# Kernel tuning notes

Measured on AMD Instinct MI355X. Metric: run time of the kernel, lower is better.

The kernel has to match this reference:

```python
import jax, jax.numpy as jnp
import numpy as np


def setup_inputs() -> dict:
    key = jax.random.key(0)
    inputs = jax.random.normal(key, (4096, 8192), dtype=jnp.float32)
    return {"inputs": inputs, "k": 512}


def reference(inputs, k):
    # Original: kth_smallest = sort_ascending(inputs)[..., n-1-k]
    # i.e. the (k+1)-th largest value per row. Equivalent via top_k.
    # Keep only elements STRICTLY greater than that threshold.
    thresh = jax.lax.top_k(inputs, k + 1)[0][..., -1]  # [batch]
    mask = (inputs > thresh[:, None]).astype(inputs.dtype)
    return inputs * mask
```

## Files before the change

kernel.cpp:

```cpp
#include <hip/hip_runtime.h>
#include <stdint.h>


constexpr int COLS = 8192;
constexpr int TPB  = 256;
constexpr int EPT  = COLS / TPB;
constexpr int VPT  = EPT / 4;
constexpr int HIST_STRIDE = 260;

__device__ __forceinline__ uint32_t map_f32(uint32_t u) {
  return (u & 0x80000000u) ? ~u : (u | 0x80000000u);
}

__device__ __forceinline__ float unmap_f32(uint32_t m) {
  return __uint_as_float((m & 0x80000000u) ? (m ^ 0x80000000u) : ~m);
}

__global__ __launch_bounds__(TPB)
void ksparse_kernel(const float* __restrict__ in, const int* __restrict__ kptr,
                    float* __restrict__ out) {
  __shared__ uint32_t hist[4 * HIST_STRIDE];
  __shared__ uint32_t sscan[256];
  __shared__ uint32_t wtot[4];
  __shared__ int s_dmax;

  const int t    = threadIdx.x;
  const int wave = t >> 6;
  const int lane = t & 63;
  const size_t rowbase = (size_t)blockIdx.x * COLS;

  uint32_t m[EPT];
  const float4* inp = (const float4*)(in + rowbase);
#pragma unroll
  for (int i = 0; i < VPT; ++i) {
    float4 v = inp[t + i * TPB];
    m[4 * i + 0] = map_f32(__float_as_uint(v.x));
    m[4 * i + 1] = map_f32(__float_as_uint(v.y));
    m[4 * i + 2] = map_f32(__float_as_uint(v.z));
    m[4 * i + 3] = map_f32(__float_as_uint(v.w));
  }

  uint32_t kk = (uint32_t)(*kptr) + 1u;
  uint32_t prefix = 0;

#pragma unroll 1
  for (int pass = 0; pass < 4; ++pass) {
    const int shift = 24 - 8 * pass;

#pragma unroll
    for (int j = 0; j < 5; ++j) {
      int idx = t + j * TPB;
      if (idx < 4 * HIST_STRIDE) hist[idx] = 0u;
    }
    if (t == 0) s_dmax = -1;
    __syncthreads();

    const uint32_t hi_mask = (pass == 0) ? 0u : (0xFFFFFFFFu << (shift + 8));
    const uint32_t want    = (pass == 0) ? 0u : (prefix << (shift + 8));
    uint32_t* h = &hist[wave * HIST_STRIDE];
#pragma unroll
    for (int i = 0; i < EPT; ++i) {
      if ((m[i] & hi_mask) == want)
        atomicAdd(&h[(m[i] >> shift) & 255u], 1u);
    }
    __syncthreads();

    uint32_t s = hist[t] + hist[HIST_STRIDE + t] +
                 hist[2 * HIST_STRIDE + t] + hist[3 * HIST_STRIDE + t];
#pragma unroll
    for (int off = 1; off < 64; off <<= 1) {
      uint32_t tmp = __shfl_down(s, off, 64);
      s += (lane + off < 64) ? tmp : 0u;
    }
    if (lane == 0) wtot[wave] = s;
    __syncthreads();

    uint32_t suff = s;
#pragma unroll
    for (int w = 1; w < 4; ++w)
      if (w > wave) suff += wtot[w];
    sscan[t] = suff;
    if (suff >= kk) atomicMax(&s_dmax, t);
    __syncthreads();

    const int d = s_dmax;
    const uint32_t above = (d < 255) ? sscan[d + 1] : 0u;
    kk -= above;
    prefix = (prefix << 8) | (uint32_t)d;
    __syncthreads();
  }

  const uint32_t T = prefix;

  float4* op = (float4*)(out + rowbase);
#pragma unroll
  for (int i = 0; i < VPT; ++i) {
    float4 v;
    uint32_t mm;
    mm  = m[4 * i + 0]; v.x = (mm > T) ? unmap_f32(mm) : 0.0f;
    mm  = m[4 * i + 1]; v.y = (mm > T) ? unmap_f32(mm) : 0.0f;
    mm  = m[4 * i + 2]; v.z = (mm > T) ? unmap_f32(mm) : 0.0f;
    mm  = m[4 * i + 3]; v.w = (mm > T) ? unmap_f32(mm) : 0.0f;
    op[t + i * TPB] = v;
  }
}

extern "C" void kernel_launch(void* const* d_in, const int* in_sizes, int n_in,
                              void* d_out, int out_size, void* d_ws, size_t ws_size,
                              hipStream_t stream) {
  const float* in  = (const float*)d_in[0];
  const int*   k   = (const int*)d_in[1];
  float*       out = (float*)d_out;
  int rows = in_sizes[0] / COLS;
  if (rows < 1) rows = 1;
  ksparse_kernel<<<rows, TPB, 0, stream>>>(in, k, out);
}
```

Baseline: 259.6 us.

## Use 3-pass 11/11/10-bit radix select with 2048-bin histograms

Replaces the four 8-bit radix-select passes with three passes of 11, 11 and 10 bits. Each pass now uses 2048-bin shared histograms with two replicas instead of four. Each thread scans 8 bins locally before the wave and block scan. This removes one full pass of histogramming, barriers and scanning. In exchange it clears larger histograms, has more atomic contention per replica, and does more scan work per thread.

New measurement: 240.1 us. 7.5% less time.

```diff
diff --git a/kernel.cpp b/kernel.cpp
--- a/kernel.cpp
+++ b/kernel.cpp
@@ -6,12 +6,12 @@
 constexpr int TPB  = 256;
 constexpr int EPT  = COLS / TPB;
 constexpr int VPT  = EPT / 4;
-constexpr int HIST_STRIDE = 260;
+constexpr int NBIN = 2048;
+constexpr int NREP = 2;
 
 __device__ __forceinline__ uint32_t map_f32(uint32_t u) {
   return (u & 0x80000000u) ? ~u : (u | 0x80000000u);
 }
-
 __device__ __forceinline__ float unmap_f32(uint32_t m) {
   return __uint_as_float((m & 0x80000000u) ? (m ^ 0x80000000u) : ~m);
 }
@@ -19,10 +19,10 @@
 __global__ __launch_bounds__(TPB)
 void ksparse_kernel(const float* __restrict__ in, const int* __restrict__ kptr,
                     float* __restrict__ out) {
-  __shared__ uint32_t hist[4 * HIST_STRIDE];
-  __shared__ uint32_t sscan[256];
+  __shared__ __align__(16) uint32_t hist[NREP * NBIN];
   __shared__ uint32_t wtot[4];
   __shared__ int s_dmax;
+  __shared__ uint32_t s_above;
 
   const int t    = threadIdx.x;
   const int wave = t >> 6;
@@ -41,32 +41,52 @@
   }
 
   uint32_t kk = (uint32_t)(*kptr) + 1u;
-  uint32_t prefix = 0;
+  uint32_t pref = 0;
+
+  const int shifts[3]  = {21, 10, 0};
+  const int dmask[3]   = {0x7FF, 0x7FF, 0x3FF};
+  const int cshifts[3] = {0, 21, 10};
 
 #pragma unroll 1
-  for (int pass = 0; pass < 4; ++pass) {
-    const int shift = 24 - 8 * pass;
+  for (int pass = 0; pass < 3; ++pass) {
+    const int shift = shifts[pass];
+    const uint32_t dm = (uint32_t)dmask[pass];
 
+    uint4* h4 = (uint4*)hist;
 #pragma unroll
-    for (int j = 0; j < 5; ++j) {
-      int idx = t + j * TPB;
-      if (idx < 4 * HIST_STRIDE) hist[idx] = 0u;
-    }
+    for (int i = 0; i < (NREP * NBIN / 4) / TPB; ++i)
+      h4[t + i * TPB] = make_uint4(0u, 0u, 0u, 0u);
     if (t == 0) s_dmax = -1;
     __syncthreads();
 
-    const uint32_t hi_mask = (pass == 0) ? 0u : (0xFFFFFFFFu << (shift + 8));
-    const uint32_t want    = (pass == 0) ? 0u : (prefix << (shift + 8));
-    uint32_t* h = &hist[wave * HIST_STRIDE];
+    uint32_t* h = &hist[(wave >> 1) * NBIN];
+    if (pass == 0) {
 #pragma unroll
-    for (int i = 0; i < EPT; ++i) {
-      if ((m[i] & hi_mask) == want)
-        atomicAdd(&h[(m[i] >> shift) & 255u], 1u);
+      for (int i = 0; i < EPT; ++i)
+        atomicAdd(&h[m[i] >> 21], 1u);
+    } else {
+      const int cs = cshifts[pass];
+#pragma unroll
+      for (int i = 0; i < EPT; ++i) {
+        if ((m[i] >> cs) == pref)
+          atomicAdd(&h[(m[i] >> shift) & dm], 1u);
+      }
     }
     __syncthreads();
 
-    uint32_t s = hist[t] + hist[HIST_STRIDE + t] +
-                 hist[2 * HIST_STRIDE + t] + hist[3 * HIST_STRIDE + t];
+    const uint4* hv = (const uint4*)hist;
+    uint4 a0 = hv[2 * t];
+    uint4 a1 = hv[2 * t + 1];
+    uint4 b0 = hv[NBIN / 4 + 2 * t];
+    uint4 b1 = hv[NBIN / 4 + 2 * t + 1];
+    uint32_t c0 = a0.x + b0.x, c1 = a0.y + b0.y, c2 = a0.z + b0.z, c3 = a0.w + b0.w;
+    uint32_t c4 = a1.x + b1.x, c5 = a1.y + b1.y, c6 = a1.z + b1.z, c7 = a1.w + b1.w;
+    uint32_t sl[8];
+    sl[7] = c7;       sl[6] = sl[7] + c6; sl[5] = sl[6] + c5; sl[4] = sl[5] + c4;
+    sl[3] = sl[4] + c3; sl[2] = sl[3] + c2; sl[1] = sl[2] + c1; sl[0] = sl[1] + c0;
+    const uint32_t total = sl[0];
+
+    uint32_t s = total;
 #pragma unroll
     for (int off = 1; off < 64; off <<= 1) {
       uint32_t tmp = __shfl_down(s, off, 64);
@@ -75,22 +95,34 @@
     if (lane == 0) wtot[wave] = s;
     __syncthreads();
 
-    uint32_t suff = s;
+    uint32_t hi = 0;
 #pragma unroll
     for (int w = 1; w < 4; ++w)
-      if (w > wave) suff += wtot[w];
-    sscan[t] = suff;
-    if (suff >= kk) atomicMax(&s_dmax, t);
+      if (w > wave) hi += wtot[w];
+    const uint32_t excl = hi + (s - total);
+
+    int best = -1;
+#pragma unroll
+    for (int j = 7; j >= 0; --j) {
+      if (best < 0 && excl + sl[j] >= kk) best = j;
+    }
+    if (best >= 0) atomicMax(&s_dmax, t * 8 + best);
     __syncthreads();
 
     const int d = s_dmax;
-    const uint32_t above = (d < 255) ? sscan[d + 1] : 0u;
-    kk -= above;
-    prefix = (prefix << 8) | (uint32_t)d;
+    if (t == (d >> 3)) {
+      const int j = d & 7;
+      s_above = excl + ((j < 7) ? sl[j + 1] : 0u);
+    }
+    __syncthreads();
+
+    kk -= s_above;
+    pref = (pass == 0) ? (uint32_t)d
+                       : ((pref << ((pass == 2) ? 10 : 11)) | (uint32_t)d);
     __syncthreads();
   }
 
-  const uint32_t T = prefix;
+  const uint32_t T = pref;
 
   float4* op = (float4*)(out + rowbase);
 #pragma unroll
```
